# Kernel tuning notes

Measured on AMD Instinct MI355X. Metric: run time of the kernel, lower is better.

The kernel has to match this reference:

```python
import jax, jax.numpy as jnp
import numpy as np

B, T, D = 4, 2048, 384
MIN_DUR = 8.0
W_SCALE = 0.02  # keeps softplus output < 8 so clamped+rounded durations are exactly 8


def setup_inputs() -> dict:
    key = jax.random.key(0)
    k_x, k_w1, k_w2 = jax.random.split(key, 3)
    x = jax.random.normal(k_x, (B, T, D), dtype=jnp.float32)
    w1 = jax.random.normal(k_w1, (D, D // 2), dtype=jnp.float32) * W_SCALE
    b1 = jnp.zeros((D // 2,), dtype=jnp.float32)
    w2 = jax.random.normal(k_w2, (D // 2, 1), dtype=jnp.float32) * W_SCALE
    b2 = jnp.zeros((1,), dtype=jnp.float32)
    total_length = B * T * int(MIN_DUR)  # == duration_pred.sum() by construction (all durs clamp to 8)
    return {"x": x, "w1": w1, "b1": b1, "w2": w2, "b2": b2, "total_length": total_length}


def reference(x, w1, b1, w2, b2, total_length):
    # 2-layer MLP duration predictor: Linear -> ReLU -> Linear -> Softplus, squeeze(-1)
    h = jax.nn.relu(jnp.einsum("btd,dh->bth", x, w1) + b1)
    duration_pred = jax.nn.softplus(jnp.einsum("bth,ho->bto", h, w2) + b2)[..., 0]  # (B, T)
    # inference path: clamp to min duration then round
    duration_pred = jnp.round(jnp.maximum(duration_pred, MIN_DUR))
    # Original expands using batch-0 durations for all rows (faithful to source).
    dur0 = duration_pred[0].astype(jnp.int32)            # (T,)
    cum = jnp.cumsum(dur0)                               # (T,) end offsets
    pos = jnp.arange(total_length)                       # static output length
    idx = jnp.minimum(jnp.searchsorted(cum, pos, side="right"), x.shape[1] - 1)
    valid = pos < cum[-1]
    # parallel gather replacing the per-timestep slice-assign loop; zeros past total fill
    expanded = jnp.where(valid[None, :, None], x[:, idx, :], jnp.zeros((), x.dtype))
    return expanded, duration_pred
```

## Files before the change

kernel.cpp:

```cpp
#include <hip/hip_runtime.h>
#include <hip/hip_bf16.h>
#include <math.h>

#define BB 4
#define TT 2048
#define DD 384
#define HH 192
#define TOTAL_LEN 65536
#define EXP_ELEMS (BB * TOTAL_LEN * DD)
#define F4_PER_ROW (DD / 4)
#define TOTAL_F4 (BB * TOTAL_LEN * F4_PER_ROW)
#define ROWS_PER_BLK 8

typedef float f32x4 __attribute__((ext_vector_type(4)));

__global__ __launch_bounds__(192) void mlp_dur_kernel(
    const float* __restrict__ x, const float* __restrict__ w1,
    const float* __restrict__ b1, const float* __restrict__ w2,
    const float* __restrict__ b2, float* __restrict__ dur_out,
    int* __restrict__ dur0) {
  __shared__ float xs[ROWS_PER_BLK * DD];
  __shared__ float part[ROWS_PER_BLK * 3];

  const int tid = threadIdx.x;
  const int lane = tid & 63;
  const int wave = tid >> 6;
  const int row0 = blockIdx.x * ROWS_PER_BLK;

  const f32x4* xg = (const f32x4*)(x + (size_t)row0 * DD);
  f32x4* xs4 = (f32x4*)xs;
#pragma unroll
  for (int i = 0; i < 4; ++i) xs4[i * 192 + tid] = xg[i * 192 + tid];
  __syncthreads();

  float acc[ROWS_PER_BLK];
#pragma unroll
  for (int r = 0; r < ROWS_PER_BLK; ++r) acc[r] = 0.f;

  const int j = tid;
  for (int k = 0; k < DD; k += 4) {
    float w[4];
#pragma unroll
    for (int kk = 0; kk < 4; ++kk) w[kk] = w1[(size_t)(k + kk) * HH + j];
#pragma unroll
    for (int r = 0; r < ROWS_PER_BLK; ++r) {
      const f32x4 xv = *(const f32x4*)(xs + r * DD + k);
#pragma unroll
      for (int kk = 0; kk < 4; ++kk) acc[r] = fmaf(xv[kk], w[kk], acc[r]);
    }
  }

  const float b1v = b1[j];
  const float w2v = w2[j];

#pragma unroll
  for (int r = 0; r < ROWS_PER_BLK; ++r) {
    float s = fmaxf(acc[r] + b1v, 0.f) * w2v;
#pragma unroll
    for (int off = 32; off > 0; off >>= 1) s += __shfl_down(s, off, 64);
    if (lane == 0) part[r * 3 + wave] = s;
  }
  __syncthreads();

  if (tid < ROWS_PER_BLK) {
    const float z = part[tid * 3] + part[tid * 3 + 1] + part[tid * 3 + 2] + b2[0];
    const float sp = fmaxf(z, 0.f) + log1pf(expf(-fabsf(z)));
    const float dur = rintf(fmaxf(sp, 8.0f));
    const int row = row0 + tid;
    dur_out[row] = dur;
    if (row < TT) dur0[row] = (int)dur;
  }
}

__global__ __launch_bounds__(256) void scan_kernel(const int* __restrict__ dur0,
                                                   int* __restrict__ cum) {
  __shared__ int lds[256];
  const int tid = threadIdx.x;
  const int base = tid * 8;
  int v[8];
  int run = 0;
#pragma unroll
  for (int i = 0; i < 8; ++i) {
    run += dur0[base + i];
    v[i] = run;
  }
  lds[tid] = run;
  __syncthreads();
  for (int off = 1; off < 256; off <<= 1) {
    const int t = (tid >= off) ? lds[tid - off] : 0;
    __syncthreads();
    lds[tid] += t;
    __syncthreads();
  }
  const int excl = lds[tid] - run;
#pragma unroll
  for (int i = 0; i < 8; ++i) cum[base + i] = v[i] + excl;
}

__global__ __launch_bounds__(256) void idx_scatter_kernel(
    const int* __restrict__ dur0, const int* __restrict__ cum,
    int* __restrict__ idx_map) {
  const int i = blockIdx.x * 256 + threadIdx.x;
  const int total = min(cum[TT - 1], TOTAL_LEN);
  if (i >= total) idx_map[i] = -1;
  if (i < TT) {
    const int end = min(cum[i], TOTAL_LEN);
    const int start = min(end, max(cum[i] - dur0[i], 0));
    for (int p = start; p < end; ++p) idx_map[p] = i;
  }
}

#define EXP_STRIDE (TOTAL_F4 / 4)
__global__ __launch_bounds__(256) void expand_kernel(
    const f32x4* __restrict__ x4, const int* __restrict__ idx_map,
    f32x4* __restrict__ out4) {
  const unsigned t = blockIdx.x * 256u + threadIdx.x;
#pragma unroll
  for (int i = 0; i < 4; ++i) {
    const unsigned e = t + (unsigned)i * EXP_STRIDE;
    const unsigned row = e / 96u;
    const unsigned col = e - row * 96u;
    const unsigned b = row >> 16;
    const unsigned pos = row & 65535u;
    const int id = idx_map[pos];
    f32x4 v = {0.f, 0.f, 0.f, 0.f};
    if (id >= 0) v = x4[((size_t)b * TT + (unsigned)id) * F4_PER_ROW + col];
    __builtin_nontemporal_store(v, out4 + e);
  }
}

extern "C" void kernel_launch(void* const* d_in, const int* in_sizes, int n_in,
                              void* d_out, int out_size, void* d_ws,
                              size_t ws_size, hipStream_t stream) {
  const float* x = (const float*)d_in[0];
  const float* w1 = (const float*)d_in[1];
  const float* b1 = (const float*)d_in[2];
  const float* w2 = (const float*)d_in[3];
  const float* b2 = (const float*)d_in[4];

  float* out = (float*)d_out;
  float* dur_out = out + (size_t)EXP_ELEMS;

  int* ws = (int*)d_ws;
  int* dur0 = ws;
  int* cum = ws + TT;
  int* idx_map = ws + 2 * TT;

  mlp_dur_kernel<<<TT * BB / ROWS_PER_BLK, 192, 0, stream>>>(x, w1, b1, w2, b2,
                                                             dur_out, dur0);
  scan_kernel<<<1, 256, 0, stream>>>(dur0, cum);
  idx_scatter_kernel<<<TOTAL_LEN / 256, 256, 0, stream>>>(dur0, cum, idx_map);
  expand_kernel<<<EXP_STRIDE / 256, 256, 0, stream>>>((const f32x4*)x, idx_map,
                                                      (f32x4*)out);
}
```

Measured before the change: 454.2 us.

## Fuse scan with scatter, drop LDS staging, simplify expand to one vector per thread

The MLP kernel drops its shared-memory staging of x and reads the input rows straight from global memory (the same address for every thread), relying on scalar or broadcast loads. The scan and index-scatter kernels are merged into one single-block kernel, which also writes the clamped total length, removing one launch and the cum buffer. The expand kernel now handles one float4 per thread with a plain store instead of four strided nontemporal stores, and tests against the total rather than a -1 sentinel. The single-block scatter serialises 2048 short write loops, and losing the nontemporal stores may change cache behaviour for the large output write.

Result: no change. 458.3 us (+0.9%).

```diff
diff --git a/kernel.cpp b/kernel.cpp
--- a/kernel.cpp
+++ b/kernel.cpp
@@ -19,34 +19,27 @@
     const float* __restrict__ b1, const float* __restrict__ w2,
     const float* __restrict__ b2, float* __restrict__ dur_out,
     int* __restrict__ dur0) {
-  __shared__ float xs[ROWS_PER_BLK * DD];
   __shared__ float part[ROWS_PER_BLK * 3];
 
   const int tid = threadIdx.x;
   const int lane = tid & 63;
   const int wave = tid >> 6;
   const int row0 = blockIdx.x * ROWS_PER_BLK;
-
-  const f32x4* xg = (const f32x4*)(x + (size_t)row0 * DD);
-  f32x4* xs4 = (f32x4*)xs;
-#pragma unroll
-  for (int i = 0; i < 4; ++i) xs4[i * 192 + tid] = xg[i * 192 + tid];
-  __syncthreads();
+  const int j = tid;
 
   float acc[ROWS_PER_BLK];
 #pragma unroll
   for (int r = 0; r < ROWS_PER_BLK; ++r) acc[r] = 0.f;
 
-  const int j = tid;
   for (int k = 0; k < DD; k += 4) {
     float w[4];
 #pragma unroll
     for (int kk = 0; kk < 4; ++kk) w[kk] = w1[(size_t)(k + kk) * HH + j];
 #pragma unroll
     for (int r = 0; r < ROWS_PER_BLK; ++r) {
-      const f32x4 xv = *(const f32x4*)(xs + r * DD + k);
+      const float* xr = x + (size_t)(row0 + r) * DD + k;
 #pragma unroll
-      for (int kk = 0; kk < 4; ++kk) acc[r] = fmaf(xv[kk], w[kk], acc[r]);
+      for (int kk = 0; kk < 4; ++kk) acc[r] = fmaf(xr[kk], w[kk], acc[r]);
     }
   }
 
@@ -72,16 +65,18 @@
   }
 }
 
-__global__ __launch_bounds__(256) void scan_kernel(const int* __restrict__ dur0,
-                                                   int* __restrict__ cum) {
+__global__ __launch_bounds__(256) void scan_scatter_kernel(
+    const int* __restrict__ dur0, int* __restrict__ idx_map,
+    int* __restrict__ total_out) {
   __shared__ int lds[256];
   const int tid = threadIdx.x;
   const int base = tid * 8;
-  int v[8];
+  int d[8], v[8];
   int run = 0;
 #pragma unroll
   for (int i = 0; i < 8; ++i) {
-    run += dur0[base + i];
+    d[i] = dur0[base + i];
+    run += d[i];
     v[i] = run;
   }
   lds[tid] = run;
@@ -93,40 +88,30 @@
     __syncthreads();
   }
   const int excl = lds[tid] - run;
+  if (tid == 255) total_out[0] = min(lds[255], TOTAL_LEN);
 #pragma unroll
-  for (int i = 0; i < 8; ++i) cum[base + i] = v[i] + excl;
-}
-
-__global__ __launch_bounds__(256) void idx_scatter_kernel(
-    const int* __restrict__ dur0, const int* __restrict__ cum,
-    int* __restrict__ idx_map) {
-  const int i = blockIdx.x * 256 + threadIdx.x;
-  const int total = min(cum[TT - 1], TOTAL_LEN);
-  if (i >= total) idx_map[i] = -1;
-  if (i < TT) {
-    const int end = min(cum[i], TOTAL_LEN);
-    const int start = min(end, max(cum[i] - dur0[i], 0));
-    for (int p = start; p < end; ++p) idx_map[p] = i;
+  for (int i = 0; i < 8; ++i) {
+    const int end = min(excl + v[i], TOTAL_LEN);
+    const int start = min(max(excl + v[i] - d[i], 0), TOTAL_LEN);
+    for (int p = start; p < end; ++p) idx_map[p] = base + i;
   }
 }
 
-#define EXP_STRIDE (TOTAL_F4 / 4)
 __global__ __launch_bounds__(256) void expand_kernel(
     const f32x4* __restrict__ x4, const int* __restrict__ idx_map,
-    f32x4* __restrict__ out4) {
+    const int* __restrict__ total_p, f32x4* __restrict__ out4) {
   const unsigned t = blockIdx.x * 256u + threadIdx.x;
-#pragma unroll
-  for (int i = 0; i < 4; ++i) {
-    const unsigned e = t + (unsigned)i * EXP_STRIDE;
-    const unsigned row = e / 96u;
-    const unsigned col = e - row * 96u;
-    const unsigned b = row >> 16;
-    const unsigned pos = row & 65535u;
+  const int total = *total_p;
+  const unsigned row = t / 96u;
+  const unsigned col = t - row * 96u;
+  const unsigned b = row >> 16;
+  const unsigned pos = row & 65535u;
+  f32x4 v = {0.f, 0.f, 0.f, 0.f};
+  if ((int)pos < total) {
     const int id = idx_map[pos];
-    f32x4 v = {0.f, 0.f, 0.f, 0.f};
-    if (id >= 0) v = x4[((size_t)b * TT + (unsigned)id) * F4_PER_ROW + col];
-    __builtin_nontemporal_store(v, out4 + e);
+    v = x4[((size_t)b * TT + (unsigned)id) * F4_PER_ROW + col];
   }
+  out4[t] = v;
 }
 
 extern "C" void kernel_launch(void* const* d_in, const int* in_sizes, int n_in,
@@ -143,13 +128,12 @@
 
   int* ws = (int*)d_ws;
   int* dur0 = ws;
-  int* cum = ws + TT;
+  int* total_p = ws + TT;
   int* idx_map = ws + 2 * TT;
 
   mlp_dur_kernel<<<TT * BB / ROWS_PER_BLK, 192, 0, stream>>>(x, w1, b1, w2, b2,
                                                              dur_out, dur0);
-  scan_kernel<<<1, 256, 0, stream>>>(dur0, cum);
-  idx_scatter_kernel<<<TOTAL_LEN / 256, 256, 0, stream>>>(dur0, cum, idx_map);
-  expand_kernel<<<EXP_STRIDE / 256, 256, 0, stream>>>((const f32x4*)x, idx_map,
-                                                      (f32x4*)out);
+  scan_scatter_kernel<<<1, 256, 0, stream>>>(dur0, idx_map, total_p);
+  expand_kernel<<<TOTAL_F4 / 256, 256, 0, stream>>>((const f32x4*)x, idx_map,
+                                                    total_p, (f32x4*)out);
 }
```
